# Optimization experiments

Measured on AMD Instinct MI355X. Metric: run time of the kernel, lower is better.

## Reference

```python
import jax, jax.numpy as jnp
import numpy as np

B, T, V, E, M, L = 1024, 64, 1024, 512, 1024, 32
PE, PO = M // 2, (M - 1) // 2  # even/odd pair counts


def complex_normalize(x, eps=1e-8):
    mag = jnp.sqrt((x.real ** 2 + x.imag ** 2).sum(-1, keepdims=True) + eps)
    return x / mag


def pair_unitary(v0, v1, t, p, r):
    # 2x2 MZI unitary applied to pairs (v0, v1); t/p/r are (P,) broadcast over batch
    c, s = jnp.cos(t), jnp.sin(t)
    eip, eir = jnp.exp(1j * p), jnp.exp(1j * r)
    u11 = eip * c * eir
    u12 = eip * (1j * s)
    u21 = (1j * s) * eir
    u22 = c
    return u11 * v0 + u12 * v1, u21 * v0 + u22 * v1


def setup_inputs() -> dict:
    key = jax.random.key(0)
    ks = jax.random.split(key, 16)
    sE = 1.0 / np.sqrt(E)
    return {
        "context_tokens": jax.random.randint(ks[0], (B, T), 0, V),
        "embed": 0.02 * jax.random.normal(ks[1], (V, E), jnp.float32),
        "W_ih": sE * jax.random.normal(ks[2], (3 * E, E), jnp.float32),
        "W_hh": sE * jax.random.normal(ks[3], (3 * E, E), jnp.float32),
        "b_ih": jnp.zeros((3 * E,), jnp.float32),
        "b_hh": jnp.zeros((3 * E,), jnp.float32),
        "Wc": 0.02 * jax.random.normal(ks[4], (2 * M, E), jnp.float32),
        "bc": jnp.zeros((2 * M,), jnp.float32),
        "phase": 0.1 * jax.random.normal(ks[5], (L, M), jnp.float32),
        "theta_e": 0.1 * jax.random.normal(ks[6], (L, PE), jnp.float32),
        "phi_e": 0.1 * jax.random.normal(ks[7], (L, PE), jnp.float32),
        "rho_e": 0.1 * jax.random.normal(ks[8], (L, PE), jnp.float32),
        "theta_o": 0.1 * jax.random.normal(ks[9], (L, PO), jnp.float32),
        "phi_o": 0.1 * jax.random.normal(ks[10], (L, PO), jnp.float32),
        "rho_o": 0.1 * jax.random.normal(ks[11], (L, PO), jnp.float32),
        "R_real": 0.01 * jax.random.normal(ks[12], (V, M), jnp.float32),
        "R_imag": 0.01 * jax.random.normal(ks[13], (V, M), jnp.float32),
    }


def reference(context_tokens, embed, W_ih, W_hh, b_ih, b_hh, Wc, bc,
              phase, theta_e, phi_e, rho_e, theta_o, phi_o, rho_o,
              R_real, R_imag):
    # --- ContextEncoder: embedding + GRU (torch gate order r,z,n) ---
    x = embed[context_tokens]                      # (B,T,E)
    x_gates = x @ W_ih.T + b_ih                    # (B,T,3E) precomputed input gates

    def gru_step(h, xg):
        ir, iz, in_ = jnp.split(xg, 3, axis=-1)
        hr, hz, hn = jnp.split(h @ W_hh.T + b_hh, 3, axis=-1)
        r = jax.nn.sigmoid(ir + hr)
        z = jax.nn.sigmoid(iz + hz)
        n = jnp.tanh(in_ + r * hn)
        return (1.0 - z) * n + z * h, None

    h0 = jnp.zeros((x.shape[0], embed.shape[1]), x.dtype)
    h, _ = jax.lax.scan(gru_step, h0, jnp.swapaxes(x_gates, 0, 1))  # (B,E)

    zc = h @ Wc.T + bc                              # (B,2M)
    re, im = jnp.split(zc, 2, axis=-1)
    psi = complex_normalize(re + 1j * im)           # (B,M) complex64

    # --- QuantumCore: stack of MZI layers ---
    def layer(psi, p):
        ph, te, pe, re_, to, po, ro = p
        psi = psi * jnp.exp(1j * ph)
        D = psi.shape[1]
        # even pairs (0,1),(2,3),...
        v0, v1 = pair_unitary(psi[:, 0::2], psi[:, 1::2], te, pe, re_)
        psi = psi.at[:, 0::2].set(v0).at[:, 1::2].set(v1)
        # odd pairs (1,2),(3,4),...
        v0, v1 = pair_unitary(psi[:, 1:D - 1:2], psi[:, 2:D:2], to, po, ro)
        psi = psi.at[:, 1:D - 1:2].set(v0).at[:, 2:D:2].set(v1)
        return complex_normalize(psi), None

    psi, _ = jax.lax.scan(layer, psi, (phase, theta_e, phi_e, rho_e,
                                       theta_o, phi_o, rho_o))

    # --- QuantumReadout: Born rule log-probs ---
    R = R_real + 1j * R_imag                        # (V,M)
    amps = psi @ R.T                                # (B,V) complex
    log_mag_sq = jnp.log(amps.real ** 2 + amps.imag ** 2 + 1e-12)
    return log_mag_sq - jax.scipy.special.logsumexp(log_mag_sq, axis=-1, keepdims=True)
```

## Files before the change

kernel.cpp:

```cpp
#include <hip/hip_runtime.h>
#include <math.h>

typedef __bf16 bf16_t;
typedef bf16_t bf16x8 __attribute__((ext_vector_type(8)));
typedef float  f32x4  __attribute__((ext_vector_type(4)));

#define B_  1024
#define T_  64
#define V_  1024
#define E_  512
#define M_  1024
#define L_  32
#define PE_ 512
#define PO_ 511
#define G3_ 1536
#define M2_ 2048

#define MFMA_BF16 __builtin_amdgcn_mfma_f32_16x16x32_bf16

__device__ __forceinline__ void stage16b(bf16_t* lds_base, const bf16_t* gsrc) {
  __builtin_amdgcn_global_load_lds(
      (const __attribute__((address_space(1))) unsigned int*)gsrc,
      (__attribute__((address_space(3))) unsigned int*)lds_base, 16, 0, 0);
}

__device__ __forceinline__ size_t tiled_off(int row, int k) {
  return ((size_t)(row >> 4) * 16 + (k >> 5)) * 512 +
         (size_t)(((k >> 3) & 3) * 16 + (row & 15)) * 8 + (k & 7);
}

__device__ __forceinline__ void split_chunk(const float* __restrict__ src,
                                            bf16_t* __restrict__ hi,
                                            bf16_t* __restrict__ lo, int blk,
                                            int tid) {
  int i4 = (blk * 256 + tid) * 4;
  float4 v = *(const float4*)&src[i4];
  float vv[4] = {v.x, v.y, v.z, v.w};
#pragma unroll
  for (int j = 0; j < 4; j++) {
    bf16_t h = (bf16_t)vv[j];
    hi[i4 + j] = h;
    lo[i4 + j] = (bf16_t)(vv[j] - (float)h);
  }
}

__global__ __launch_bounds__(256) void prep_all(
    const float* __restrict__ embed, bf16_t* __restrict__ emb_hi,
    bf16_t* __restrict__ emb_lo, const float* __restrict__ W_ih,
    bf16_t* __restrict__ wih_hi, bf16_t* __restrict__ wih_lo,
    const float* __restrict__ Wc, bf16_t* __restrict__ wc_hi,
    bf16_t* __restrict__ wc_lo, const float* __restrict__ R_real,
    bf16_t* __restrict__ rr_hi, bf16_t* __restrict__ rr_lo,
    const float* __restrict__ R_imag, bf16_t* __restrict__ ri_hi,
    bf16_t* __restrict__ ri_lo, const float* __restrict__ W_hh,
    bf16_t* __restrict__ Wp_hi, bf16_t* __restrict__ Wp_lo,
    const float* __restrict__ phase, const float* __restrict__ th_e,
    const float* __restrict__ ph_e, const float* __restrict__ rh_e,
    float* __restrict__ Uep, const float* __restrict__ th_o,
    const float* __restrict__ ph_o, const float* __restrict__ rh_o,
    float* __restrict__ Uop) {
  const int bid = blockIdx.x, tid = threadIdx.x;
  if (bid < 512) {
    split_chunk(embed, emb_hi, emb_lo, bid, tid);
  } else if (bid < 1280) {
    split_chunk(W_ih, wih_hi, wih_lo, bid - 512, tid);
  } else if (bid < 2304) {
    split_chunk(Wc, wc_hi, wc_lo, bid - 1280, tid);
  } else if (bid < 3328) {
    split_chunk(R_real, rr_hi, rr_lo, bid - 2304, tid);
  } else if (bid < 4352) {
    split_chunk(R_imag, ri_hi, ri_lo, bid - 3328, tid);
  } else if (bid < 5888) {
    int q = bid - 4352;
    int c = q / 96, loc = q % 96;
    int g = loc >> 5, el = loc & 31;
    const float* src = &W_hh[(size_t)(g * 512 + c * 32 + el) * 512];
    if (tid < 64) {
      int k0 = tid * 8;
      float4 v0 = *(const float4*)&src[k0];
      float4 v1 = *(const float4*)&src[k0 + 4];
      float vv[8] = {v0.x, v0.y, v0.z, v0.w, v1.x, v1.y, v1.z, v1.w};
      bf16x8 h8, l8;
#pragma unroll
      for (int j = 0; j < 8; j++) {
        bf16_t h = (bf16_t)vv[j];
        h8[j] = h;
        l8[j] = (bf16_t)(vv[j] - (float)h);
      }
      size_t toff = tiled_off(q, k0);
      *(bf16x8*)&Wp_hi[toff] = h8;
      *(bf16x8*)&Wp_lo[toff] = l8;
    }
  } else if (bid < 5952) {
    int idx = (bid - 5888) * 256 + tid;
    if (idx < L_ * PE_) {
      int l = idx >> 9, p = idx & 511;
      float t = th_e[idx], pp = ph_e[idx], r = rh_e[idx];
      float c = cosf(t), s = sinf(t);
      float cp = cosf(pp), sp = sinf(pp), cr = cosf(r), sr = sinf(r);
      float u11r = c * (cp * cr - sp * sr), u11i = c * (cp * sr + sp * cr);
      float u12r = -s * sp, u12i = s * cp;
      float u21r = -s * sr, u21i = s * cr;
      float u22r = c, u22i = 0.0f;
      float f0 = phase[l * M_ + 2 * p], f1 = phase[l * M_ + 2 * p + 1];
      float c0 = cosf(f0), s0 = sinf(f0), c1 = cosf(f1), s1 = sinf(f1);
      float a, b;
      a = u11r * c0 - u11i * s0; b = u11r * s0 + u11i * c0; u11r = a; u11i = b;
      a = u21r * c0 - u21i * s0; b = u21r * s0 + u21i * c0; u21r = a; u21i = b;
      a = u12r * c1 - u12i * s1; b = u12r * s1 + u12i * c1; u12r = a; u12i = b;
      a = u22r * c1 - u22i * s1; b = u22r * s1 + u22i * c1; u22r = a; u22i = b;
      int j = p & 3, ln = (p >> 2) & 63, hh = p >> 8;
      size_t base = (size_t)l * 4096 + (size_t)(j * 4 + hh) * 256 + ln * 4;
      *(float4*)&Uep[base]       = make_float4(u11r, u11i, u12r, u12i);
      *(float4*)&Uep[base + 512] = make_float4(u21r, u21i, u22r, u22i);
    }
  } else {
    int idx = (bid - 5952) * 256 + tid;
    if (idx < L_ * PO_) {
      int l = idx / PO_, p = idx % PO_;
      float t = th_o[idx], pp = ph_o[idx], r = rh_o[idx];
      float c = cosf(t), s = sinf(t);
      float cp = cosf(pp), sp = sinf(pp), cr = cosf(r), sr = sinf(r);
      int j = p & 3, ln = (p >> 2) & 63, hh = p >> 8;
      size_t base = (size_t)l * 4096 + (size_t)(j * 4 + hh) * 256 + ln * 4;
      *(float4*)&Uop[base] = make_float4(c * (cp * cr - sp * sr),
                                         c * (cp * sr + sp * cr), -s * sp,
                                         s * cp);
      *(float4*)&Uop[base + 512] = make_float4(-s * sr, s * cr, c, 0.0f);
    }
  }
}

__global__ __launch_bounds__(256) void gemm_bt_mfma_split(
    const bf16_t* __restrict__ Ah, const bf16_t* __restrict__ Al,
    const bf16_t* __restrict__ Bh, const bf16_t* __restrict__ Bl,
    float* __restrict__ C, int Ndim, int K) {
  __shared__ bf16_t sAh[64 * 32], sAl[64 * 32], sBh[64 * 32], sBl[64 * 32];
  const int tid = threadIdx.x;
  const int m0 = blockIdx.y * 64, n0 = blockIdx.x * 64;
  const int wave = tid >> 6, lane = tid & 63;
  const int wr = wave >> 1, wc = wave & 1;
  const int quad = lane >> 4, l16 = lane & 15;
  f32x4 acc[2][2] = {};
  const int srow = tid >> 2, sk = (tid & 3) * 8;

  for (int k0 = 0; k0 < K; k0 += 32) {
    bf16x8 ah = *(const bf16x8*)&Ah[(size_t)(m0 + srow) * K + k0 + sk];
    bf16x8 al = *(const bf16x8*)&Al[(size_t)(m0 + srow) * K + k0 + sk];
    bf16x8 bh = *(const bf16x8*)&Bh[(size_t)(n0 + srow) * K + k0 + sk];
    bf16x8 bl = *(const bf16x8*)&Bl[(size_t)(n0 + srow) * K + k0 + sk];
    __syncthreads();
    *(bf16x8*)&sAh[srow * 32 + sk] = ah;
    *(bf16x8*)&sAl[srow * 32 + sk] = al;
    *(bf16x8*)&sBh[srow * 32 + sk] = bh;
    *(bf16x8*)&sBl[srow * 32 + sk] = bl;
    __syncthreads();
    bf16x8 fAh[2], fAl[2], fBh[2], fBl[2];
#pragma unroll
    for (int i = 0; i < 2; i++) {
      fAh[i] = *(const bf16x8*)&sAh[(wr * 32 + i * 16 + l16) * 32 + quad * 8];
      fAl[i] = *(const bf16x8*)&sAl[(wr * 32 + i * 16 + l16) * 32 + quad * 8];
      fBh[i] = *(const bf16x8*)&sBh[(wc * 32 + i * 16 + l16) * 32 + quad * 8];
      fBl[i] = *(const bf16x8*)&sBl[(wc * 32 + i * 16 + l16) * 32 + quad * 8];
    }
#pragma unroll
    for (int i = 0; i < 2; i++)
#pragma unroll
      for (int j = 0; j < 2; j++) {
        acc[i][j] = MFMA_BF16(fAh[i], fBh[j], acc[i][j], 0, 0, 0);
        acc[i][j] = MFMA_BF16(fAh[i], fBl[j], acc[i][j], 0, 0, 0);
        acc[i][j] = MFMA_BF16(fAl[i], fBh[j], acc[i][j], 0, 0, 0);
      }
  }
#pragma unroll
  for (int i = 0; i < 2; i++)
#pragma unroll
    for (int j = 0; j < 2; j++)
#pragma unroll
      for (int r = 0; r < 4; r++) {
        int row = wr * 32 + i * 16 + quad * 4 + r;
        int col = wc * 32 + j * 16 + l16;
        C[(size_t)(m0 + row) * Ndim + n0 + col] = acc[i][j][r];
      }
}

__global__ __launch_bounds__(512) void gru_step11(
    const bf16_t* __restrict__ Hh, const bf16_t* __restrict__ Hl,
    const bf16_t* __restrict__ Wph, const bf16_t* __restrict__ Wpl,
    const int* __restrict__ tok, const float* __restrict__ eg,
    const float* __restrict__ b_ih, const float* __restrict__ b_hh,
    bf16_t* __restrict__ Oh, bf16_t* __restrict__ Ol, int t, int final_) {
  __shared__ bf16_t sB[2][2][24 * 512];
  __shared__ float sC[2][64 * 100];
  __shared__ float sbih[96], sbhh[96];
  const int tid = threadIdx.x;
  const int g = tid >> 8;
  const int gtid = tid & 255;
  const int ct = blockIdx.y, m0 = blockIdx.x * 64;
  const int n0e = ct * 32;
  const int wg = gtid >> 6, lane = tid & 63;
  const int wr = wg >> 1, wc = wg & 1;
  const int quad = lane >> 4, l16 = lane & 15;

#define STAGE_B(buf, it)                                                      \
  {                                                                           \
    _Pragma("unroll") for (int r = 0; r < 6; r++) {                           \
      int c = wg * 6 + r;                                                     \
      int f = (c >= 12) ? (c - 12) : c;                                       \
      int j = f >> 1, ks = f & 1;                                             \
      const bf16_t* srcp = (c < 12) ? Wph : Wpl;                              \
      stage16b(&sB[buf][g][c * 512],                                          \
               &srcp[(size_t)(ct * 6 + j) * 8192 +                            \
                     (size_t)(g * 8 + (it) * 2 + ks) * 512 + lane * 8]);      \
    }                                                                         \
  }

  STAGE_B(0, 0);

  if (tid < 96) {
    sbih[tid] = b_ih[(tid >> 5) * 512 + n0e + (tid & 31)];
    sbhh[tid] = b_hh[(tid >> 5) * 512 + n0e + (tid & 31)];
  }

  float pir[4], piz[4], pin[4], phv[4];
#pragma unroll
  for (int u = 0; u < 4; u++) {
    int flat = u * 512 + tid;
    int row = flat >> 5, el = flat & 31;
    int bb = m0 + row, eG = n0e + el;
    int tk = tok[bb * T_ + t];
    pir[u] = eg[(size_t)tk * G3_ + eG];
    piz[u] = eg[(size_t)tk * G3_ + 512 + eG];
    pin[u] = eg[(size_t)tk * G3_ + 1024 + eG];
    size_t toff = tiled_off(bb, eG);
    phv[u] = (float)Hh[toff] + (float)Hl[toff];
  }

  const size_t aB0 = (size_t)((m0 >> 4) + wr * 2 + 0) * 8192 + (size_t)g * 4096 + lane * 8;
  const size_t aB1 = (size_t)((m0 >> 4) + wr * 2 + 1) * 8192 + (size_t)g * 4096 + lane * 8;

  f32x4 acc[2][3] = {};
  __syncthreads();
#pragma unroll
  for (int it = 0; it < 4; ++it) {
    const int buf = it & 1;
    if (it < 3) STAGE_B(buf ^ 1, it + 1);
    const bf16_t* sBg = &sB[buf][g][0];
#pragma unroll
    for (int ks2 = 0; ks2 < 2; ++ks2) {
      const int kb = it * 2 + ks2;
      const int ko = kb * 512;
      bf16x8 fah[2], fal[2], fbh[3], fbl[3];
      fah[0] = *(const bf16x8*)&Hh[aB0 + ko];
      fah[1] = *(const bf16x8*)&Hh[aB1 + ko];
      fal[0] = *(const bf16x8*)&Hl[aB0 + ko];
      fal[1] = *(const bf16x8*)&Hl[aB1 + ko];
#pragma unroll
      for (int j = 0; j < 3; j++) {
        int f = (wc * 3 + j) * 2 + ks2;
        fbh[j] = *(const bf16x8*)&sBg[f * 512 + lane * 8];
        fbl[j] = *(const bf16x8*)&sBg[(f + 12) * 512 + lane * 8];
      }
#pragma unroll
      for (int i = 0; i < 2; i++)
#pragma unroll
        for (int j = 0; j < 3; j++) {
          acc[i][j] = MFMA_BF16(fah[i], fbh[j], acc[i][j], 0, 0, 0);
          acc[i][j] = MFMA_BF16(fah[i], fbl[j], acc[i][j], 0, 0, 0);
          acc[i][j] = MFMA_BF16(fal[i], fbh[j], acc[i][j], 0, 0, 0);
        }
    }
    __syncthreads();
  }
#undef STAGE_B
#pragma unroll
  for (int i = 0; i < 2; i++)
#pragma unroll
    for (int j = 0; j < 3; j++)
#pragma unroll
      for (int r = 0; r < 4; r++)
        sC[g][(wr * 32 + i * 16 + quad * 4 + r) * 100 + wc * 48 + j * 16 + l16] =
            acc[i][j][r];
  __syncthreads();
#pragma unroll
  for (int u = 0; u < 4; u++) {
    int flat = u * 512 + tid;
    int row = flat >> 5, el = flat & 31;
    int bb = m0 + row, eG = n0e + el;
    float ir = pir[u] + sbih[el];
    float iz = piz[u] + sbih[32 + el];
    float in_ = pin[u] + sbih[64 + el];
    float hr = sC[0][row * 100 + el] + sC[1][row * 100 + el] + sbhh[el];
    float hz = sC[0][row * 100 + 32 + el] + sC[1][row * 100 + 32 + el] + sbhh[32 + el];
    float hn = sC[0][row * 100 + 64 + el] + sC[1][row * 100 + 64 + el] + sbhh[64 + el];
    float r = 1.0f / (1.0f + __expf(-(ir + hr)));
    float z = 1.0f / (1.0f + __expf(-(iz + hz)));
    float targ = fminf(fmaxf(in_ + r * hn, -15.0f), 15.0f);
    float e2 = __expf(2.0f * targ);
    float n = (e2 - 1.0f) / (e2 + 1.0f);
    float hnew = (1.0f - z) * n + z * phv[u];
    bf16_t hh = (bf16_t)hnew;
    bf16_t ll = (bf16_t)(hnew - (float)hh);
    if (final_) {
      size_t hidx = (size_t)bb * 512 + eG;
      Oh[hidx] = hh;
      Ol[hidx] = ll;
    } else {
      size_t toff = tiled_off(bb, eG);
      Oh[toff] = hh;
      Ol[toff] = ll;
    }
  }
}

__device__ inline void apply_u(float4 A, float4 Bv, float& x0r, float& x0i,
                               float& x1r, float& x1i) {
  float n0r = A.x * x0r - A.y * x0i + A.z * x1r - A.w * x1i;
  float n0i = A.x * x0i + A.y * x0r + A.z * x1i + A.w * x1r;
  float n1r = Bv.x * x0r - Bv.y * x0i + Bv.z * x1r - Bv.w * x1i;
  float n1i = Bv.x * x0i + Bv.y * x0r + Bv.z * x1i + Bv.w * x1r;
  x0r = n0r; x0i = n0i; x1r = n1r; x1i = n1i;
}

__global__ __launch_bounds__(256) void qc7(
    const float* __restrict__ zc, const float* __restrict__ bc,
    const float* __restrict__ Uep, const float* __restrict__ Uop,
    bf16_t* __restrict__ prh, bf16_t* __restrict__ prl,
    bf16_t* __restrict__ pih, bf16_t* __restrict__ pil) {
  __shared__ float sred[4];
  __shared__ float4 sEx[2][2][2];
  const int tid = threadIdx.x;
  const int wave = tid >> 6, lane = tid & 63;
  const int wb = wave >> 1, h = wave & 1;
  const int b = blockIdx.x * 2 + wb;
  const int e0 = h * 512 + lane * 8;

  float xr[8], xi[8];
  {
    const float4* zr4 = (const float4*)&zc[(size_t)b * M2_ + e0];
    const float4* zi4 = (const float4*)&zc[(size_t)b * M2_ + M_ + e0];
    const float4* br4 = (const float4*)&bc[e0];
    const float4* bi4 = (const float4*)&bc[M_ + e0];
#pragma unroll
    for (int q = 0; q < 2; q++) {
      float4 a = zr4[q], bb = br4[q];
      xr[4 * q + 0] = a.x + bb.x; xr[4 * q + 1] = a.y + bb.y;
      xr[4 * q + 2] = a.z + bb.z; xr[4 * q + 3] = a.w + bb.w;
      float4 c2 = zi4[q], d = bi4[q];
      xi[4 * q + 0] = c2.x + d.x; xi[4 * q + 1] = c2.y + d.y;
      xi[4 * q + 2] = c2.z + d.z; xi[4 * q + 3] = c2.w + d.w;
    }
  }
  {
    float s = 0.0f;
#pragma unroll
    for (int k = 0; k < 8; k++) s += xr[k] * xr[k] + xi[k] * xi[k];
    for (int off = 32; off; off >>= 1) s += __shfl_xor(s, off);
    if (lane == 0) sred[wave] = s;
    __syncthreads();
    float inv = 1.0f / sqrtf(sred[2 * wb] + sred[2 * wb + 1] + 1e-8f);
#pragma unroll
    for (int k = 0; k < 8; k++) { xr[k] *= inv; xi[k] *= inv; }
  }
  if (h == 0 && lane == 63) sEx[0][wb][0] = make_float4(xr[6], xi[6], xr[7], xi[7]);
  if (h == 1 && lane == 0)  sEx[0][wb][1] = make_float4(xr[0], xi[0], xr[1], xi[1]);
  __syncthreads();

#pragma unroll 1
  for (int l = 0; l < L_; ++l) {
    const int buf = l & 1;
    const float* Ub = &Uep[(size_t)l * 4096];
    const float* Ob = &Uop[(size_t)l * 4096];
    float4 eA[4], eB[4], oA[3], oB[3], A3, B3;
#pragma unroll
    for (int j = 0; j < 4; j++) {
      eA[j] = *(const float4*)&Ub[(j * 4 + h) * 256 + lane * 4];
      eB[j] = *(const float4*)&Ub[(j * 4 + 2 + h) * 256 + lane * 4];
    }
#pragma unroll
    for (int j = 0; j < 3; j++) {
      oA[j] = *(const float4*)&Ob[(j * 4 + h) * 256 + lane * 4];
      oB[j] = *(const float4*)&Ob[(j * 4 + 2 + h) * 256 + lane * 4];
    }
    A3 = *(const float4*)&Ob[(12 + h) * 256 + lane * 4];
    B3 = *(const float4*)&Ob[(14 + h) * 256 + lane * 4];
    float4 par = make_float4(0.f, 0.f, 0.f, 0.f);
    if (h == 0 && lane == 63) par = sEx[buf][wb][1];
    if (h == 1 && lane == 0)  par = sEx[buf][wb][0];
#pragma unroll
    for (int j = 0; j < 4; j++)
      apply_u(eA[j], eB[j], xr[2 * j], xi[2 * j], xr[2 * j + 1], xi[2 * j + 1]);
    float exr = 0.f, exi = 0.f;
    if (h == 0 && lane == 63) {
      float4 Ae = *(const float4*)&Ub[1 * 256];
      exr = Ae.x * par.x - Ae.y * par.y + Ae.z * par.z - Ae.w * par.w;
      exi = Ae.x * par.y + Ae.y * par.x + Ae.z * par.w + Ae.w * par.z;
    }
    if (h == 1 && lane == 0) {
      float4 Be = *(const float4*)&Ub[14 * 256 + 252];
      exr = Be.x * par.x - Be.y * par.y + Be.z * par.z - Be.w * par.w;
      exi = Be.x * par.y + Be.y * par.x + Be.z * par.w + Be.w * par.z;
    }
#pragma unroll
    for (int j = 0; j < 3; j++)
      apply_u(oA[j], oB[j], xr[2 * j + 1], xi[2 * j + 1], xr[2 * j + 2],
              xi[2 * j + 2]);
    float nr = __shfl_down(xr[0], 1), ni = __shfl_down(xi[0], 1);
    if (h == 0 && lane == 63) { nr = exr; ni = exi; }
    float srr = 0.f, sii = 0.f;
    if (!(h == 1 && lane == 63)) {
      float n0r = A3.x * xr[7] - A3.y * xi[7] + A3.z * nr - A3.w * ni;
      float n0i = A3.x * xi[7] + A3.y * xr[7] + A3.z * ni + A3.w * nr;
      srr = B3.x * xr[7] - B3.y * xi[7] + B3.z * nr - B3.w * ni;
      sii = B3.x * xi[7] + B3.y * xr[7] + B3.z * ni + B3.w * nr;
      xr[7] = n0r; xi[7] = n0i;
    }
    float nx0r = 0.f, nx0i = 0.f;
    if (h == 1 && lane == 0) {
      float4 Bc = *(const float4*)&Ob[14 * 256 + 252];
      nx0r = Bc.x * exr - Bc.y * exi + Bc.z * xr[0] - Bc.w * xi[0];
      nx0i = Bc.x * exi + Bc.y * exr + Bc.z * xi[0] + Bc.w * xr[0];
    }
    float rr = __shfl_up(srr, 1), ri2 = __shfl_up(sii, 1);
    if (lane > 0) { xr[0] = rr; xi[0] = ri2; }
    if (h == 1 && lane == 0) { xr[0] = nx0r; xi[0] = nx0i; }
    if (h == 0 && lane == 63)
      sEx[1 - buf][wb][0] = make_float4(xr[6], xi[6], xr[7], xi[7]);
    if (h == 1 && lane == 0)
      sEx[1 - buf][wb][1] = make_float4(xr[0], xi[0], xr[1], xi[1]);
    __syncthreads();
  }
  size_t base = (size_t)b * M_ + e0;
  bf16x8 vh, vl, wh, wl;
#pragma unroll
  for (int k = 0; k < 8; k++) {
    float vr = xr[k], vi = xi[k];
    bf16_t h1 = (bf16_t)vr;
    vh[k] = h1; vl[k] = (bf16_t)(vr - (float)h1);
    bf16_t h2 = (bf16_t)vi;
    wh[k] = h2; wl[k] = (bf16_t)(vi - (float)h2);
  }
  *(bf16x8*)&prh[base] = vh;
  *(bf16x8*)&prl[base] = vl;
  *(bf16x8*)&pih[base] = wh;
  *(bf16x8*)&pil[base] = wl;
}

__global__ __launch_bounds__(256) void readout_mfma(
    const bf16_t* __restrict__ Arh, const bf16_t* __restrict__ Arl,
    const bf16_t* __restrict__ Aih, const bf16_t* __restrict__ Ail,
    const bf16_t* __restrict__ Brh, const bf16_t* __restrict__ Brl,
    const bf16_t* __restrict__ Bih, const bf16_t* __restrict__ Bil,
    float* __restrict__ out) {
  __shared__ bf16_t sArh[64 * 32], sArl[64 * 32], sAih[64 * 32], sAil[64 * 32];
  __shared__ bf16_t sBrh[64 * 32], sBrl[64 * 32], sBih[64 * 32], sBil[64 * 32];
  const int tid = threadIdx.x;
  const int b0 = blockIdx.y * 64, v0 = blockIdx.x * 64;
  const int wave = tid >> 6, lane = tid & 63;
  const int wr = wave >> 1, wc = wave & 1;
  const int quad = lane >> 4, l16 = lane & 15;
  f32x4 aP[2][2] = {}, aQ[2][2] = {}, aI[2][2] = {};
  const int srow = tid >> 2, sk = (tid & 3) * 8;

  for (int k0 = 0; k0 < M_; k0 += 32) {
    size_t aoff = (size_t)(b0 + srow) * M_ + k0 + sk;
    size_t boff = (size_t)(v0 + srow) * M_ + k0 + sk;
    bf16x8 v0r = *(const bf16x8*)&Arh[aoff];
    bf16x8 v1r = *(const bf16x8*)&Arl[aoff];
    bf16x8 v2r = *(const bf16x8*)&Aih[aoff];
    bf16x8 v3r = *(const bf16x8*)&Ail[aoff];
    bf16x8 v4r = *(const bf16x8*)&Brh[boff];
    bf16x8 v5r = *(const bf16x8*)&Brl[boff];
    bf16x8 v6r = *(const bf16x8*)&Bih[boff];
    bf16x8 v7r = *(const bf16x8*)&Bil[boff];
    __syncthreads();
    *(bf16x8*)&sArh[srow * 32 + sk] = v0r;
    *(bf16x8*)&sArl[srow * 32 + sk] = v1r;
    *(bf16x8*)&sAih[srow * 32 + sk] = v2r;
    *(bf16x8*)&sAil[srow * 32 + sk] = v3r;
    *(bf16x8*)&sBrh[srow * 32 + sk] = v4r;
    *(bf16x8*)&sBrl[srow * 32 + sk] = v5r;
    *(bf16x8*)&sBih[srow * 32 + sk] = v6r;
    *(bf16x8*)&sBil[srow * 32 + sk] = v7r;
    __syncthreads();
    bf16x8 fArh[2], fArl[2], fAih[2], fAil[2], fBrh[2], fBrl[2], fBih[2], fBil[2];
#pragma unroll
    for (int i = 0; i < 2; i++) {
      int ra = (wr * 32 + i * 16 + l16) * 32 + quad * 8;
      int rb = (wc * 32 + i * 16 + l16) * 32 + quad * 8;
      fArh[i] = *(const bf16x8*)&sArh[ra];
      fArl[i] = *(const bf16x8*)&sArl[ra];
      fAih[i] = *(const bf16x8*)&sAih[ra];
      fAil[i] = *(const bf16x8*)&sAil[ra];
      fBrh[i] = *(const bf16x8*)&sBrh[rb];
      fBrl[i] = *(const bf16x8*)&sBrl[rb];
      fBih[i] = *(const bf16x8*)&sBih[rb];
      fBil[i] = *(const bf16x8*)&sBil[rb];
    }
#pragma unroll
    for (int i = 0; i < 2; i++)
#pragma unroll
      for (int j = 0; j < 2; j++) {
        aP[i][j] = MFMA_BF16(fArh[i], fBrh[j], aP[i][j], 0, 0, 0);
        aP[i][j] = MFMA_BF16(fArh[i], fBrl[j], aP[i][j], 0, 0, 0);
        aP[i][j] = MFMA_BF16(fArl[i], fBrh[j], aP[i][j], 0, 0, 0);
        aQ[i][j] = MFMA_BF16(fAih[i], fBih[j], aQ[i][j], 0, 0, 0);
        aQ[i][j] = MFMA_BF16(fAih[i], fBil[j], aQ[i][j], 0, 0, 0);
        aQ[i][j] = MFMA_BF16(fAil[i], fBih[j], aQ[i][j], 0, 0, 0);
        aI[i][j] = MFMA_BF16(fArh[i], fBih[j], aI[i][j], 0, 0, 0);
        aI[i][j] = MFMA_BF16(fArh[i], fBil[j], aI[i][j], 0, 0, 0);
        aI[i][j] = MFMA_BF16(fArl[i], fBih[j], aI[i][j], 0, 0, 0);
        aI[i][j] = MFMA_BF16(fAih[i], fBrh[j], aI[i][j], 0, 0, 0);
        aI[i][j] = MFMA_BF16(fAih[i], fBrl[j], aI[i][j], 0, 0, 0);
        aI[i][j] = MFMA_BF16(fAil[i], fBrh[j], aI[i][j], 0, 0, 0);
      }
  }
#pragma unroll
  for (int i = 0; i < 2; i++)
#pragma unroll
    for (int j = 0; j < 2; j++)
#pragma unroll
      for (int r = 0; r < 4; r++) {
        int row = wr * 32 + i * 16 + quad * 4 + r;
        int col = wc * 32 + j * 16 + l16;
        float re = aP[i][j][r] - aQ[i][j][r];
        float im = aI[i][j][r];
        out[(size_t)(b0 + row) * V_ + v0 + col] = logf(re * re + im * im + 1e-12f);
      }
}

__global__ __launch_bounds__(256) void lse_kernel(float* __restrict__ out) {
  __shared__ float redm[4], reds[4];
  const int b = blockIdx.x, t = threadIdx.x;
  float4 v = *(float4*)&out[(size_t)b * V_ + 4 * t];
  float mx = fmaxf(fmaxf(v.x, v.y), fmaxf(v.z, v.w));
  for (int off = 32; off; off >>= 1) mx = fmaxf(mx, __shfl_down(mx, off, 64));
  if ((t & 63) == 0) redm[t >> 6] = mx;
  __syncthreads();
  mx = fmaxf(fmaxf(redm[0], redm[1]), fmaxf(redm[2], redm[3]));
  float s = expf(v.x - mx) + expf(v.y - mx) + expf(v.z - mx) + expf(v.w - mx);
  for (int off = 32; off; off >>= 1) s += __shfl_down(s, off, 64);
  if ((t & 63) == 0) reds[t >> 6] = s;
  __syncthreads();
  s = reds[0] + reds[1] + reds[2] + reds[3];
  float lse = mx + logf(s);
  v.x -= lse; v.y -= lse; v.z -= lse; v.w -= lse;
  *(float4*)&out[(size_t)b * V_ + 4 * t] = v;
}

extern "C" void kernel_launch(void* const* d_in, const int* in_sizes, int n_in,
                              void* d_out, int out_size, void* d_ws, size_t ws_size,
                              hipStream_t stream) {
  const int*   tokens = (const int*)d_in[0];
  const float* embed  = (const float*)d_in[1];
  const float* W_ih   = (const float*)d_in[2];
  const float* W_hh   = (const float*)d_in[3];
  const float* b_ih   = (const float*)d_in[4];
  const float* b_hh   = (const float*)d_in[5];
  const float* Wc     = (const float*)d_in[6];
  const float* bc     = (const float*)d_in[7];
  const float* phase  = (const float*)d_in[8];
  const float* theta_e = (const float*)d_in[9];
  const float* phi_e  = (const float*)d_in[10];
  const float* rho_e  = (const float*)d_in[11];
  const float* theta_o = (const float*)d_in[12];
  const float* phi_o  = (const float*)d_in[13];
  const float* rho_o  = (const float*)d_in[14];
  const float* R_real = (const float*)d_in[15];
  const float* R_imag = (const float*)d_in[16];
  float* out = (float*)d_out;

  char* w = (char*)d_ws;
  auto alloc = [&](size_t bytes) -> void* {
    void* p = (void*)w;
    w += (bytes + 255) & ~(size_t)255;
    return p;
  };
  char* region0 = w;
  bf16_t* emb_hi = (bf16_t*)alloc((size_t)V_ * E_ * 2);
  bf16_t* emb_lo = (bf16_t*)alloc((size_t)V_ * E_ * 2);
  bf16_t* wih_hi = (bf16_t*)alloc((size_t)G3_ * E_ * 2);
  bf16_t* wih_lo = (bf16_t*)alloc((size_t)G3_ * E_ * 2);
  bf16_t* wc_hi  = (bf16_t*)alloc((size_t)M2_ * E_ * 2);
  bf16_t* wc_lo  = (bf16_t*)alloc((size_t)M2_ * E_ * 2);
  char* region1 = w;
  float*  eg     = (float*)alloc((size_t)V_ * G3_ * 4);
  bf16_t* Wp_hi  = (bf16_t*)alloc((size_t)G3_ * E_ * 2);
  bf16_t* Wp_lo  = (bf16_t*)alloc((size_t)G3_ * E_ * 2);
  bf16_t* h0_hi = (bf16_t*)alloc((size_t)B_ * E_ * 2);
  bf16_t* h0_lo = (bf16_t*)alloc((size_t)B_ * E_ * 2);
  bf16_t* h1_hi = (bf16_t*)alloc((size_t)B_ * E_ * 2);
  bf16_t* h1_lo = (bf16_t*)alloc((size_t)B_ * E_ * 2);
  bf16_t* rr_hi = (bf16_t*)alloc((size_t)V_ * M_ * 2);
  bf16_t* rr_lo = (bf16_t*)alloc((size_t)V_ * M_ * 2);
  bf16_t* ri_hi = (bf16_t*)alloc((size_t)V_ * M_ * 2);
  bf16_t* ri_lo = (bf16_t*)alloc((size_t)V_ * M_ * 2);
  float*  Uep   = (float*)alloc((size_t)L_ * 4096 * 4);
  float*  Uop   = (float*)alloc((size_t)L_ * 4096 * 4);

  float*  zc  = (float*)region1;
  bf16_t* prh = (bf16_t*)(region0 + 0 * 2097152);
  bf16_t* prl = (bf16_t*)(region0 + 1 * 2097152);
  bf16_t* pih = (bf16_t*)(region0 + 2 * 2097152);
  bf16_t* pil = (bf16_t*)(region0 + 3 * 2097152);

  hipMemsetAsync(h0_hi, 0, (size_t)B_ * E_ * 2 * 2, stream);

  prep_all<<<6016, 256, 0, stream>>>(
      embed, emb_hi, emb_lo, W_ih, wih_hi, wih_lo, Wc, wc_hi, wc_lo, R_real,
      rr_hi, rr_lo, R_imag, ri_hi, ri_lo, W_hh, Wp_hi, Wp_lo, phase, theta_e,
      phi_e, rho_e, Uep, theta_o, phi_o, rho_o, Uop);

  {
    dim3 grid(G3_ / 64, V_ / 64);
    gemm_bt_mfma_split<<<grid, 256, 0, stream>>>(emb_hi, emb_lo, wih_hi, wih_lo,
                                                 eg, G3_, E_);
  }

  for (int t = 0; t < T_; ++t) {
    const bf16_t* ih = (t & 1) ? h1_hi : h0_hi;
    const bf16_t* il = (t & 1) ? h1_lo : h0_lo;
    bf16_t* oh = (t & 1) ? h0_hi : h1_hi;
    bf16_t* ol = (t & 1) ? h0_lo : h1_lo;
    dim3 grid(16, 16);
    gru_step11<<<grid, 512, 0, stream>>>(ih, il, Wp_hi, Wp_lo, tokens, eg,
                                         b_ih, b_hh, oh, ol, t,
                                         (t == T_ - 1) ? 1 : 0);
  }

  {
    dim3 grid(M2_ / 64, B_ / 64);
    gemm_bt_mfma_split<<<grid, 256, 0, stream>>>(h0_hi, h0_lo, wc_hi, wc_lo,
                                                 zc, M2_, E_);
  }

  qc7<<<B_ / 2, 256, 0, stream>>>(zc, bc, Uep, Uop, prh, prl, pih, pil);

  {
    dim3 grid(V_ / 64, B_ / 64);
    readout_mfma<<<grid, 256, 0, stream>>>(prh, prl, pih, pil, rr_hi, rr_lo,
                                           ri_hi, ri_lo, out);
  }

  lse_kernel<<<B_, 256, 0, stream>>>(out);
}
```

Measured before the change: 842.3 us.

## Run quantum core with one wave per two batch rows, no LDS sync

The MZI layer kernel now gives one 64-lane wave two batch rows, with each lane holding 16 elements per row. Before, a row was split across two waves that traded boundary elements through shared memory and __syncthreads. The unitary tables are repacked so each lane reads 8 consecutive pair coefficients, and those loaded coefficients are reused for both rows. This removes block-wide barriers and halves coefficient loads per row. In exchange it uses about 64 state floats per lane plus coefficient registers, and only 512 single-wave blocks run, which lowers parallelism and latency hiding.

```diff
diff --git a/kernel.cpp b/kernel.cpp
--- a/kernel.cpp
+++ b/kernel.cpp
@@ -109,10 +109,10 @@
       a = u21r * c0 - u21i * s0; b = u21r * s0 + u21i * c0; u21r = a; u21i = b;
       a = u12r * c1 - u12i * s1; b = u12r * s1 + u12i * c1; u12r = a; u12i = b;
       a = u22r * c1 - u22i * s1; b = u22r * s1 + u22i * c1; u22r = a; u22i = b;
-      int j = p & 3, ln = (p >> 2) & 63, hh = p >> 8;
-      size_t base = (size_t)l * 4096 + (size_t)(j * 4 + hh) * 256 + ln * 4;
+      int j = p & 7, ln = p >> 3;
+      size_t base = (size_t)l * 4096 + (size_t)(2 * j) * 256 + ln * 4;
       *(float4*)&Uep[base]       = make_float4(u11r, u11i, u12r, u12i);
-      *(float4*)&Uep[base + 512] = make_float4(u21r, u21i, u22r, u22i);
+      *(float4*)&Uep[base + 256] = make_float4(u21r, u21i, u22r, u22i);
     }
   } else {
     int idx = (bid - 5952) * 256 + tid;
@@ -121,12 +121,12 @@
       float t = th_o[idx], pp = ph_o[idx], r = rh_o[idx];
       float c = cosf(t), s = sinf(t);
       float cp = cosf(pp), sp = sinf(pp), cr = cosf(r), sr = sinf(r);
-      int j = p & 3, ln = (p >> 2) & 63, hh = p >> 8;
-      size_t base = (size_t)l * 4096 + (size_t)(j * 4 + hh) * 256 + ln * 4;
+      int j = p & 7, ln = p >> 3;
+      size_t base = (size_t)l * 4096 + (size_t)(2 * j) * 256 + ln * 4;
       *(float4*)&Uop[base] = make_float4(c * (cp * cr - sp * sr),
                                          c * (cp * sr + sp * cr), -s * sp,
                                          s * cp);
-      *(float4*)&Uop[base + 512] = make_float4(-s * sr, s * cr, c, 0.0f);
+      *(float4*)&Uop[base + 256] = make_float4(-s * sr, s * cr, c, 0.0f);
     }
   }
 }
@@ -322,128 +322,134 @@
   x0r = n0r; x0i = n0i; x1r = n1r; x1i = n1i;
 }
 
-__global__ __launch_bounds__(256) void qc7(
+__global__ __launch_bounds__(64) void qc8(
     const float* __restrict__ zc, const float* __restrict__ bc,
     const float* __restrict__ Uep, const float* __restrict__ Uop,
     bf16_t* __restrict__ prh, bf16_t* __restrict__ prl,
     bf16_t* __restrict__ pih, bf16_t* __restrict__ pil) {
-  __shared__ float sred[4];
-  __shared__ float4 sEx[2][2][2];
-  const int tid = threadIdx.x;
-  const int wave = tid >> 6, lane = tid & 63;
-  const int wb = wave >> 1, h = wave & 1;
-  const int b = blockIdx.x * 2 + wb;
-  const int e0 = h * 512 + lane * 8;
-
-  float xr[8], xi[8];
-  {
-    const float4* zr4 = (const float4*)&zc[(size_t)b * M2_ + e0];
-    const float4* zi4 = (const float4*)&zc[(size_t)b * M2_ + M_ + e0];
-    const float4* br4 = (const float4*)&bc[e0];
-    const float4* bi4 = (const float4*)&bc[M_ + e0];
-#pragma unroll
-    for (int q = 0; q < 2; q++) {
-      float4 a = zr4[q], bb = br4[q];
-      xr[4 * q + 0] = a.x + bb.x; xr[4 * q + 1] = a.y + bb.y;
-      xr[4 * q + 2] = a.z + bb.z; xr[4 * q + 3] = a.w + bb.w;
-      float4 c2 = zi4[q], d = bi4[q];
-      xi[4 * q + 0] = c2.x + d.x; xi[4 * q + 1] = c2.y + d.y;
-      xi[4 * q + 2] = c2.z + d.z; xi[4 * q + 3] = c2.w + d.w;
-    }
-  }
-  {
-    float s = 0.0f;
-#pragma unroll
-    for (int k = 0; k < 8; k++) s += xr[k] * xr[k] + xi[k] * xi[k];
-    for (int off = 32; off; off >>= 1) s += __shfl_xor(s, off);
-    if (lane == 0) sred[wave] = s;
-    __syncthreads();
-    float inv = 1.0f / sqrtf(sred[2 * wb] + sred[2 * wb + 1] + 1e-8f);
-#pragma unroll
-    for (int k = 0; k < 8; k++) { xr[k] *= inv; xi[k] *= inv; }
-  }
-  if (h == 0 && lane == 63) sEx[0][wb][0] = make_float4(xr[6], xi[6], xr[7], xi[7]);
-  if (h == 1 && lane == 0)  sEx[0][wb][1] = make_float4(xr[0], xi[0], xr[1], xi[1]);
-  __syncthreads();
+  const int lane = threadIdx.x;
+  const int b0 = blockIdx.x * 2, b1 = b0 + 1;
+  const int e0 = lane * 16;
+
+  float xr0[16], xi0[16], xr1[16], xi1[16];
+#define LOAD_B(bb, xr, xi)                                                    \
+  {                                                                           \
+    const float4* zr4 = (const float4*)&zc[(size_t)(bb) * M2_ + e0];          \
+    const float4* zi4 = (const float4*)&zc[(size_t)(bb) * M2_ + M_ + e0];     \
+    const float4* br4 = (const float4*)&bc[e0];                               \
+    const float4* bi4 = (const float4*)&bc[M_ + e0];                          \
+    _Pragma("unroll") for (int q = 0; q < 4; q++) {                           \
+      float4 a = zr4[q], b4 = br4[q];                                         \
+      xr[4 * q + 0] = a.x + b4.x; xr[4 * q + 1] = a.y + b4.y;                 \
+      xr[4 * q + 2] = a.z + b4.z; xr[4 * q + 3] = a.w + b4.w;                 \
+      float4 c4 = zi4[q], d4 = bi4[q];                                        \
+      xi[4 * q + 0] = c4.x + d4.x; xi[4 * q + 1] = c4.y + d4.y;               \
+      xi[4 * q + 2] = c4.z + d4.z; xi[4 * q + 3] = c4.w + d4.w;               \
+    }                                                                         \
+  }
+  LOAD_B(b0, xr0, xi0);
+  LOAD_B(b1, xr1, xi1);
+#undef LOAD_B
+
+#define NORM_B(xr, xi)                                                        \
+  {                                                                           \
+    float s = 0.0f;                                                           \
+    _Pragma("unroll") for (int k = 0; k < 16; k++)                            \
+        s += xr[k] * xr[k] + xi[k] * xi[k];                                   \
+    for (int off = 32; off; off >>= 1) s += __shfl_xor(s, off);               \
+    float inv = 1.0f / sqrtf(s + 1e-8f);                                      \
+    _Pragma("unroll") for (int k = 0; k < 16; k++) {                          \
+      xr[k] *= inv; xi[k] *= inv;                                             \
+    }                                                                         \
+  }
+  NORM_B(xr0, xi0);
+  NORM_B(xr1, xi1);
+#undef NORM_B
 
 #pragma unroll 1
   for (int l = 0; l < L_; ++l) {
-    const int buf = l & 1;
     const float* Ub = &Uep[(size_t)l * 4096];
     const float* Ob = &Uop[(size_t)l * 4096];
-    float4 eA[4], eB[4], oA[3], oB[3], A3, B3;
-#pragma unroll
-    for (int j = 0; j < 4; j++) {
-      eA[j] = *(const float4*)&Ub[(j * 4 + h) * 256 + lane * 4];
-      eB[j] = *(const float4*)&Ub[(j * 4 + 2 + h) * 256 + lane * 4];
-    }
-#pragma unroll
-    for (int j = 0; j < 3; j++) {
-      oA[j] = *(const float4*)&Ob[(j * 4 + h) * 256 + lane * 4];
-      oB[j] = *(const float4*)&Ob[(j * 4 + 2 + h) * 256 + lane * 4];
-    }
-    A3 = *(const float4*)&Ob[(12 + h) * 256 + lane * 4];
-    B3 = *(const float4*)&Ob[(14 + h) * 256 + lane * 4];
-    float4 par = make_float4(0.f, 0.f, 0.f, 0.f);
-    if (h == 0 && lane == 63) par = sEx[buf][wb][1];
-    if (h == 1 && lane == 0)  par = sEx[buf][wb][0];
-#pragma unroll
-    for (int j = 0; j < 4; j++)
-      apply_u(eA[j], eB[j], xr[2 * j], xi[2 * j], xr[2 * j + 1], xi[2 * j + 1]);
-    float exr = 0.f, exi = 0.f;
-    if (h == 0 && lane == 63) {
-      float4 Ae = *(const float4*)&Ub[1 * 256];
-      exr = Ae.x * par.x - Ae.y * par.y + Ae.z * par.z - Ae.w * par.w;
-      exi = Ae.x * par.y + Ae.y * par.x + Ae.z * par.w + Ae.w * par.z;
-    }
-    if (h == 1 && lane == 0) {
-      float4 Be = *(const float4*)&Ub[14 * 256 + 252];
-      exr = Be.x * par.x - Be.y * par.y + Be.z * par.z - Be.w * par.w;
-      exi = Be.x * par.y + Be.y * par.x + Be.z * par.w + Be.w * par.z;
-    }
-#pragma unroll
-    for (int j = 0; j < 3; j++)
-      apply_u(oA[j], oB[j], xr[2 * j + 1], xi[2 * j + 1], xr[2 * j + 2],
-              xi[2 * j + 2]);
-    float nr = __shfl_down(xr[0], 1), ni = __shfl_down(xi[0], 1);
-    if (h == 0 && lane == 63) { nr = exr; ni = exi; }
-    float srr = 0.f, sii = 0.f;
-    if (!(h == 1 && lane == 63)) {
-      float n0r = A3.x * xr[7] - A3.y * xi[7] + A3.z * nr - A3.w * ni;
-      float n0i = A3.x * xi[7] + A3.y * xr[7] + A3.z * ni + A3.w * nr;
-      srr = B3.x * xr[7] - B3.y * xi[7] + B3.z * nr - B3.w * ni;
-      sii = B3.x * xi[7] + B3.y * xr[7] + B3.z * ni + B3.w * nr;
-      xr[7] = n0r; xi[7] = n0i;
-    }
-    float nx0r = 0.f, nx0i = 0.f;
-    if (h == 1 && lane == 0) {
-      float4 Bc = *(const float4*)&Ob[14 * 256 + 252];
-      nx0r = Bc.x * exr - Bc.y * exi + Bc.z * xr[0] - Bc.w * xi[0];
-      nx0i = Bc.x * exi + Bc.y * exr + Bc.z * xi[0] + Bc.w * xr[0];
-    }
-    float rr = __shfl_up(srr, 1), ri2 = __shfl_up(sii, 1);
-    if (lane > 0) { xr[0] = rr; xi[0] = ri2; }
-    if (h == 1 && lane == 0) { xr[0] = nx0r; xi[0] = nx0i; }
-    if (h == 0 && lane == 63)
-      sEx[1 - buf][wb][0] = make_float4(xr[6], xi[6], xr[7], xi[7]);
-    if (h == 1 && lane == 0)
-      sEx[1 - buf][wb][1] = make_float4(xr[0], xi[0], xr[1], xi[1]);
-    __syncthreads();
-  }
-  size_t base = (size_t)b * M_ + e0;
-  bf16x8 vh, vl, wh, wl;
-#pragma unroll
-  for (int k = 0; k < 8; k++) {
-    float vr = xr[k], vi = xi[k];
-    bf16_t h1 = (bf16_t)vr;
-    vh[k] = h1; vl[k] = (bf16_t)(vr - (float)h1);
-    bf16_t h2 = (bf16_t)vi;
-    wh[k] = h2; wl[k] = (bf16_t)(vi - (float)h2);
-  }
-  *(bf16x8*)&prh[base] = vh;
-  *(bf16x8*)&prl[base] = vl;
-  *(bf16x8*)&pih[base] = wh;
-  *(bf16x8*)&pil[base] = wl;
+    {
+      float4 eA[8], eB[8];
+#pragma unroll
+      for (int j = 0; j < 8; j++) {
+        eA[j] = *(const float4*)&Ub[(2 * j) * 256 + lane * 4];
+        eB[j] = *(const float4*)&Ub[(2 * j + 1) * 256 + lane * 4];
+      }
+#pragma unroll
+      for (int j = 0; j < 8; j++) {
+        apply_u(eA[j], eB[j], xr0[2 * j], xi0[2 * j], xr0[2 * j + 1],
+                xi0[2 * j + 1]);
+        apply_u(eA[j], eB[j], xr1[2 * j], xi1[2 * j], xr1[2 * j + 1],
+                xi1[2 * j + 1]);
+      }
+    }
+    {
+      float4 oA[8], oB[8];
+#pragma unroll
+      for (int j = 0; j < 8; j++) {
+        oA[j] = *(const float4*)&Ob[(2 * j) * 256 + lane * 4];
+        oB[j] = *(const float4*)&Ob[(2 * j + 1) * 256 + lane * 4];
+      }
+      float nr0 = __shfl_down(xr0[0], 1), ni0 = __shfl_down(xi0[0], 1);
+      float nr1 = __shfl_down(xr1[0], 1), ni1 = __shfl_down(xi1[0], 1);
+#pragma unroll
+      for (int j = 0; j < 7; j++) {
+        apply_u(oA[j], oB[j], xr0[2 * j + 1], xi0[2 * j + 1], xr0[2 * j + 2],
+                xi0[2 * j + 2]);
+        apply_u(oA[j], oB[j], xr1[2 * j + 1], xi1[2 * j + 1], xr1[2 * j + 2],
+                xi1[2 * j + 2]);
+      }
+      float s0r = 0.f, s0i = 0.f, s1r = 0.f, s1i = 0.f;
+      if (lane < 63) {
+        {
+          float4 A = oA[7], Bv = oB[7];
+          float n0r = A.x * xr0[15] - A.y * xi0[15] + A.z * nr0 - A.w * ni0;
+          float n0i = A.x * xi0[15] + A.y * xr0[15] + A.z * ni0 + A.w * nr0;
+          s0r = Bv.x * xr0[15] - Bv.y * xi0[15] + Bv.z * nr0 - Bv.w * ni0;
+          s0i = Bv.x * xi0[15] + Bv.y * xr0[15] + Bv.z * ni0 + Bv.w * nr0;
+          xr0[15] = n0r; xi0[15] = n0i;
+        }
+        {
+          float4 A = oA[7], Bv = oB[7];
+          float n0r = A.x * xr1[15] - A.y * xi1[15] + A.z * nr1 - A.w * ni1;
+          float n0i = A.x * xi1[15] + A.y * xr1[15] + A.z * ni1 + A.w * nr1;
+          s1r = Bv.x * xr1[15] - Bv.y * xi1[15] + Bv.z * nr1 - Bv.w * ni1;
+          s1i = Bv.x * xi1[15] + Bv.y * xr1[15] + Bv.z * ni1 + Bv.w * nr1;
+          xr1[15] = n0r; xi1[15] = n0i;
+        }
+      }
+      float r0 = __shfl_up(s0r, 1), i0 = __shfl_up(s0i, 1);
+      float r1 = __shfl_up(s1r, 1), i1 = __shfl_up(s1i, 1);
+      if (lane > 0) {
+        xr0[0] = r0; xi0[0] = i0;
+        xr1[0] = r1; xi1[0] = i1;
+      }
+    }
+  }
+
+#define STORE_B(bb, xr, xi)                                                   \
+  {                                                                           \
+    size_t base = (size_t)(bb) * M_ + e0;                                     \
+    _Pragma("unroll") for (int half = 0; half < 2; half++) {                  \
+      bf16x8 vh, vl, wh, wl;                                                  \
+      _Pragma("unroll") for (int k = 0; k < 8; k++) {                         \
+        float vr = xr[half * 8 + k], vi = xi[half * 8 + k];                   \
+        bf16_t h1 = (bf16_t)vr;                                               \
+        vh[k] = h1; vl[k] = (bf16_t)(vr - (float)h1);                         \
+        bf16_t h2 = (bf16_t)vi;                                               \
+        wh[k] = h2; wl[k] = (bf16_t)(vi - (float)h2);                         \
+      }                                                                       \
+      *(bf16x8*)&prh[base + half * 8] = vh;                                   \
+      *(bf16x8*)&prl[base + half * 8] = vl;                                   \
+      *(bf16x8*)&pih[base + half * 8] = wh;                                   \
+      *(bf16x8*)&pil[base + half * 8] = wl;                                   \
+    }                                                                         \
+  }
+  STORE_B(b0, xr0, xi0);
+  STORE_B(b1, xr1, xi1);
+#undef STORE_B
 }
 
 __global__ __launch_bounds__(256) void readout_mfma(
@@ -634,7 +640,7 @@
                                                  zc, M2_, E_);
   }
 
-  qc7<<<B_ / 2, 256, 0, stream>>>(zc, bc, Uep, Uop, prh, prl, pih, pil);
+  qc8<<<B_ / 2, 64, 0, stream>>>(zc, bc, Uep, Uop, prh, prl, pih, pil);
 
   {
     dim3 grid(V_ / 64, B_ / 64);
```

Measured after the change: 966.4 us. +14.7%, slower.
